# Performance work log

Hardware: AMD Instinct MI355X
Metric: run time of the kernel (lower is better)

The kernel has to match this reference:

```python
import jax, jax.numpy as jnp
import numpy as np

D_IN = 1024
D_OUT = 1024
N, S = 4, 2048

def setup_inputs() -> dict:
    key = jax.random.key(0)
    kv, kk, kq, k1, k2, k3 = jax.random.split(key, 6)
    return {
        "v": jax.random.normal(kv, (N, S, D_IN), dtype=jnp.float32),
        "k": jax.random.normal(kk, (N, S, D_IN), dtype=jnp.float32),
        "q": jax.random.normal(kq, (N, S, D_IN), dtype=jnp.float32),
        "WV": jax.random.normal(k1, (D_OUT, D_IN), dtype=jnp.float32),
        "WQ": jax.random.normal(k2, (D_OUT, D_IN), dtype=jnp.float32),
        "WK": jax.random.normal(k3, (D_OUT, D_IN), dtype=jnp.float32),
    }

def reference(v, k, q, WV, WQ, WK) -> jnp.ndarray:
    # projections: x @ W.T  -> [N, S, D_OUT]
    wv = jnp.einsum('nsw,ow->nso', v, WV)
    wk = jnp.einsum('nsw,ow->nso', k, WK)
    wq = jnp.einsum('nsw,ow->nso', q, WQ)
    # scores [N, Sq, Sk]; NOTE: softmax over axis=1 (query axis, matching torch dim=1),
    # then post-hoc division by input_shape[0] AFTER softmax (faithful to source).
    scores = jnp.einsum('nqo,nko->nqk', wq, wk)
    wqk = jax.nn.softmax(scores, axis=1) / jnp.float32(D_IN)
    return jnp.einsum('nqk,nko->nqo', wqk, wv)
```

## Files before the change

kernel.cpp:

```cpp
#include <hip/hip_runtime.h>
#include <math.h>


typedef _Float16 f16;
typedef _Float16 f16x8 __attribute__((ext_vector_type(8)));
typedef _Float16 f16x4 __attribute__((ext_vector_type(4)));
typedef float f32x4 __attribute__((ext_vector_type(4)));

enum StageMode { SM_PLANES2, SM_PLANES1 };
enum EpiMode   { EPI_F32, EPI_SPLIT, EPI_F16T };

#define GLL_PITCH 32

__device__ __forceinline__ void gll16(const f16* g, f16* l) {
    __builtin_amdgcn_global_load_lds(
        (const __attribute__((address_space(1))) void*)g,
        (__attribute__((address_space(3))) void*)l, 16, 0, 0);
}

__device__ __forceinline__ void stage_gll_plane(const f16* __restrict__ gplane,
                                                f16* __restrict__ lds,
                                                long rowBase, int ld, int k0,
                                                int wave, int lane)
{
#pragma unroll
    for (int i = 0; i < 2; i++) {
        int slotBase = (wave * 2 + i) * 64;
        int t = slotBase + lane;
        int r = t >> 2;
        int c = (t & 3) ^ ((r >> 1) & 3);
        const f16* g = gplane + (rowBase + r) * (long)ld + k0 + c * 8;
        gll16(g, lds + (long)slotBase * 8);
    }
}

__device__ __forceinline__ int frag_off_gll(int row, int g) {
    return row * GLL_PITCH + ((g ^ ((row >> 1) & 3)) << 3);
}

template<StageMode SA, StageMode SB, EpiMode EP, int GROUPM, bool STATS>
__global__ __launch_bounds__(256, 4)
void mfma_gemm(const f16* __restrict__ Ahi, const f16* __restrict__ Alo,
               const f16* __restrict__ Bhi, const f16* __restrict__ Blo,
               float* __restrict__ pmOut, float* __restrict__ psOut,
               void* __restrict__ C0, void* __restrict__ C1,
               int M, int Nc, int K, int lda, int ldb, int ldc,
               long batchA, long batchB, long batchC,
               float epiScale, int tsShift)
{
    constexpr bool TRIPLE = (SA == SM_PLANES2);
    constexpr int PLANE_SZ = 128 * GLL_PITCH;

    int bx, by;
    if constexpr (GROUPM > 0) {
        int gx = gridDim.x;
        int lin = blockIdx.y * gx + blockIdx.x;
        int nig = GROUPM * gx;
        int gid = lin / nig;
        int rem = lin - gid * nig;
        by = gid * GROUPM + (rem % GROUPM);
        bx = rem / GROUPM;
    } else {
        bx = blockIdx.x;
        by = blockIdx.y;
    }
    const int n0 = bx * 128;
    const int m0 = by * 128;
    const long z = blockIdx.z;

    const long aOfs = z * batchA, bOfs = z * batchB, cOfs = z * batchC;

    __shared__ __align__(16) f16 As_hi[PLANE_SZ];
    __shared__ __align__(16) f16 Bs_hi[PLANE_SZ];
    __shared__ __align__(16) f16 As_lo[TRIPLE ? PLANE_SZ : 8];
    __shared__ __align__(16) f16 Bs_lo[TRIPLE ? PLANE_SZ : 8];

    const int tid  = threadIdx.x;
    const int lane = tid & 63;
    const int wave = tid >> 6;
    const int wr = (wave >> 1) * 64;
    const int wc = (wave & 1) * 64;
    const int fm = lane & 15;
    const int fg = lane >> 4;

    f32x4 acc[4][4];
#pragma unroll
    for (int i = 0; i < 4; i++)
#pragma unroll
        for (int j = 0; j < 4; j++) acc[i][j] = (f32x4){0.f, 0.f, 0.f, 0.f};

    int roA[4], roB[4];
#pragma unroll
    for (int i = 0; i < 4; i++) {
        roA[i] = frag_off_gll(wr + i * 16 + fm, fg);
        roB[i] = frag_off_gll(wc + i * 16 + fm, fg);
    }

    for (int k0 = 0; k0 < K; k0 += 32) {
        stage_gll_plane(Ahi + aOfs, As_hi, m0, lda, k0, wave, lane);
        stage_gll_plane(Bhi + bOfs, Bs_hi, n0, ldb, k0, wave, lane);
        if constexpr (TRIPLE) {
            stage_gll_plane(Alo + aOfs, As_lo, m0, lda, k0, wave, lane);
            stage_gll_plane(Blo + bOfs, Bs_lo, n0, ldb, k0, wave, lane);
        }
        __syncthreads();

        f16x8 ah[4], bh[4], al[4], bl[4];
#pragma unroll
        for (int i = 0; i < 4; i++) {
            ah[i] = *(const f16x8*)&As_hi[roA[i]];
            bh[i] = *(const f16x8*)&Bs_hi[roB[i]];
            if constexpr (TRIPLE) {
                al[i] = *(const f16x8*)&As_lo[roA[i]];
                bl[i] = *(const f16x8*)&Bs_lo[roB[i]];
            }
        }
#pragma unroll
        for (int i = 0; i < 4; i++) {
#pragma unroll
            for (int j = 0; j < 4; j++) {
                acc[i][j] = __builtin_amdgcn_mfma_f32_16x16x32_f16(ah[i], bh[j], acc[i][j], 0, 0, 0);
                if constexpr (TRIPLE) {
                    acc[i][j] = __builtin_amdgcn_mfma_f32_16x16x32_f16(ah[i], bl[j], acc[i][j], 0, 0, 0);
                    acc[i][j] = __builtin_amdgcn_mfma_f32_16x16x32_f16(al[i], bh[j], acc[i][j], 0, 0, 0);
                }
            }
        }
        __syncthreads();
    }

    const int cr = fg * 4;
    const int cn = fm;
#pragma unroll
    for (int i = 0; i < 4; i++) {
#pragma unroll
        for (int j = 0; j < 4; j++) {
#pragma unroll
            for (int r = 0; r < 4; r++) {
                long mg = m0 + wr + i * 16 + cr + r;
                long ng = n0 + wc + j * 16 + cn;
                float val = acc[i][j][r] * epiScale;
                if constexpr (EP == EPI_F32) {
                    ((float*)C0)[cOfs + mg * ldc + ng] = val;
                } else if constexpr (EP == EPI_SPLIT) {
                    f16 h = (f16)val;
                    ((f16*)C0)[cOfs + mg * ldc + ng] = h;
                    ((f16*)C1)[cOfs + mg * ldc + ng] = (f16)(val - (float)h);
                } else {
                    long TS = 1L << tsShift;
                    long nb = mg >> tsShift;
                    long s  = mg & (TS - 1);
                    long addr = nb * ((long)Nc << tsShift) + ng * TS + s;
                    ((f16*)C0)[addr] = (f16)val;
                }
            }
        }
    }

    if constexpr (STATS) {
        __shared__ float stM[2][128];
        __shared__ float stS[2][128];
#pragma unroll
        for (int j = 0; j < 4; j++) {
            float mj = -3.402823466e38f;
#pragma unroll
            for (int i = 0; i < 4; i++)
#pragma unroll
                for (int r = 0; r < 4; r++) mj = fmaxf(mj, acc[i][j][r]);
            float sj = 0.f;
#pragma unroll
            for (int i = 0; i < 4; i++)
#pragma unroll
                for (int r = 0; r < 4; r++) sj += __expf(acc[i][j][r] - mj);
#pragma unroll
            for (int mask = 16; mask <= 32; mask <<= 1) {
                float mo = __shfl_xor(mj, mask, 64);
                float so = __shfl_xor(sj, mask, 64);
                float mn = fmaxf(mj, mo);
                sj = sj * __expf(mj - mn) + so * __expf(mo - mn);
                mj = mn;
            }
            if (fg == 0) {
                stM[wave >> 1][wc + j * 16 + cn] = mj;
                stS[wave >> 1][wc + j * 16 + cn] = sj;
            }
        }
        __syncthreads();
        if (tid < 128) {
            float ma = stM[0][tid], mb = stM[1][tid];
            float Mc = fmaxf(ma, mb);
            float Sv = stS[0][tid] * __expf(ma - Mc) + stS[1][tid] * __expf(mb - Mc);
            long o = ((long)z * (M >> 7) + by) * (long)Nc + (long)bx * 128 + tid;
            pmOut[o] = Mc;
            psOut[o] = Sv;
        }
    }
}

__global__ __launch_bounds__(512, 2)
void scores_gemm(const f16* __restrict__ Ahi, const f16* __restrict__ Alo,
                 const f16* __restrict__ Bhi, const f16* __restrict__ Blo,
                 float* __restrict__ pmOut, float* __restrict__ psOut,
                 float* __restrict__ C,
                 int M, int Nc, int K, int lda, int ldb, int ldc,
                 long batchA, long batchB, long batchC)
{
    constexpr int PLANE = 256 * GLL_PITCH;

    __shared__ __align__(16) f16 As_hi[2][PLANE];
    __shared__ __align__(16) f16 As_lo[2][PLANE];
    __shared__ __align__(16) f16 Bs_hi[2][PLANE];
    __shared__ __align__(16) f16 Bs_lo[2][PLANE];

    const int tid  = threadIdx.x;
    const int lane = tid & 63;
    const int wave = tid >> 6;
    const int rw   = wave >> 2;
    const int cw   = wave & 3;
    const int wrM  = rw * 128;
    const int wrN  = cw * 64;
    const int fm   = lane & 15;
    const int fg   = lane >> 4;

    const int n0 = blockIdx.x * 256;
    const int m0 = blockIdx.y * 256;
    const long z = blockIdx.z;
    const long aOfs = z * batchA, bOfs = z * batchB, cOfs = z * batchC;

    int slotBase[2], srcA[2], srcB[2];
#pragma unroll
    for (int i = 0; i < 2; i++) {
        int sb = (wave * 2 + i) * 64;
        int t  = sb + lane;
        int r  = t >> 2;
        int c  = (t & 3) ^ ((r >> 1) & 3);
        slotBase[i] = sb * 8;
        srcA[i] = (m0 + r) * lda + c * 8;
        srcB[i] = (n0 + r) * ldb + c * 8;
    }

#define SC_STAGE(buf, k0) do {                                              \
    _Pragma("unroll")                                                        \
    for (int s_ = 0; s_ < 2; s_++) {                                         \
        gll16(Ahi + aOfs + srcA[s_] + (k0), &As_hi[buf][slotBase[s_]]);      \
        gll16(Alo + aOfs + srcA[s_] + (k0), &As_lo[buf][slotBase[s_]]);      \
        gll16(Bhi + bOfs + srcB[s_] + (k0), &Bs_hi[buf][slotBase[s_]]);      \
        gll16(Blo + bOfs + srcB[s_] + (k0), &Bs_lo[buf][slotBase[s_]]);      \
    } } while (0)

    f32x4 acc[8][4];
#pragma unroll
    for (int i = 0; i < 8; i++)
#pragma unroll
        for (int j = 0; j < 4; j++) acc[i][j] = (f32x4){0.f, 0.f, 0.f, 0.f};

    int roA[8], roB[4];
#pragma unroll
    for (int i = 0; i < 8; i++) roA[i] = frag_off_gll(wrM + i * 16 + fm, fg);
#pragma unroll
    for (int j = 0; j < 4; j++) roB[j] = frag_off_gll(wrN + j * 16 + fm, fg);

    const int NT = K >> 5;
    SC_STAGE(0, 0);

    for (int t = 0; t < NT; t++) {
        const int cur = t & 1;
        __syncthreads();
        if (t + 1 < NT) SC_STAGE(cur ^ 1, (t + 1) * 32);

        f16x8 bh[4], bl[4];
#pragma unroll
        for (int j = 0; j < 4; j++) {
            bh[j] = *(const f16x8*)&Bs_hi[cur][roB[j]];
            bl[j] = *(const f16x8*)&Bs_lo[cur][roB[j]];
        }
#pragma unroll
        for (int h = 0; h < 2; h++) {
            f16x8 ah[4], al[4];
#pragma unroll
            for (int i = 0; i < 4; i++) {
                ah[i] = *(const f16x8*)&As_hi[cur][roA[h * 4 + i]];
                al[i] = *(const f16x8*)&As_lo[cur][roA[h * 4 + i]];
            }
            __builtin_amdgcn_s_setprio(1);
#pragma unroll
            for (int i = 0; i < 4; i++)
#pragma unroll
                for (int j = 0; j < 4; j++)
                    acc[h * 4 + i][j] = __builtin_amdgcn_mfma_f32_16x16x32_f16(
                        ah[i], bh[j], acc[h * 4 + i][j], 0, 0, 0);
#pragma unroll
            for (int i = 0; i < 4; i++)
#pragma unroll
                for (int j = 0; j < 4; j++)
                    acc[h * 4 + i][j] = __builtin_amdgcn_mfma_f32_16x16x32_f16(
                        ah[i], bl[j], acc[h * 4 + i][j], 0, 0, 0);
#pragma unroll
            for (int i = 0; i < 4; i++)
#pragma unroll
                for (int j = 0; j < 4; j++)
                    acc[h * 4 + i][j] = __builtin_amdgcn_mfma_f32_16x16x32_f16(
                        al[i], bh[j], acc[h * 4 + i][j], 0, 0, 0);
            __builtin_amdgcn_s_setprio(0);
        }
    }
#undef SC_STAGE

    const int cr = fg * 4;
#pragma unroll
    for (int i = 0; i < 8; i++) {
#pragma unroll
        for (int j = 0; j < 4; j++) {
#pragma unroll
            for (int r = 0; r < 4; r++) {
                long mg = m0 + wrM + i * 16 + cr + r;
                long ng = n0 + wrN + j * 16 + fm;
                C[cOfs + mg * (long)ldc + ng] = acc[i][j][r];
            }
        }
    }

    __shared__ float stM[2][256];
    __shared__ float stS[2][256];
#pragma unroll
    for (int j = 0; j < 4; j++) {
        float mj = -3.402823466e38f;
#pragma unroll
        for (int i = 0; i < 8; i++)
#pragma unroll
            for (int r = 0; r < 4; r++) mj = fmaxf(mj, acc[i][j][r]);
        float sj = 0.f;
#pragma unroll
        for (int i = 0; i < 8; i++)
#pragma unroll
            for (int r = 0; r < 4; r++) sj += __expf(acc[i][j][r] - mj);
#pragma unroll
        for (int mask = 16; mask <= 32; mask <<= 1) {
            float mo = __shfl_xor(mj, mask, 64);
            float so = __shfl_xor(sj, mask, 64);
            float mn = fmaxf(mj, mo);
            sj = sj * __expf(mj - mn) + so * __expf(mo - mn);
            mj = mn;
        }
        if (fg == 0) {
            stM[rw][wrN + j * 16 + fm] = mj;
            stS[rw][wrN + j * 16 + fm] = sj;
        }
    }
    __syncthreads();
    if (tid < 256) {
        float ma = stM[0][tid], mb = stM[1][tid];
        float Mc = fmaxf(ma, mb);
        float Sv = stS[0][tid] * __expf(ma - Mc) + stS[1][tid] * __expf(mb - Mc);
        long o = ((long)z * (M >> 8) + blockIdx.y) * (long)Nc + (long)blockIdx.x * 256 + tid;
        pmOut[o] = Mc;
        psOut[o] = Sv;
    }
}

template<bool HAS_LO>
__global__ __launch_bounds__(256)
void split_kernel(const float* __restrict__ src, f16* __restrict__ hi,
                  f16* __restrict__ lo, long n)
{
    long i = ((long)blockIdx.x * 256 + threadIdx.x) * 8;
    if (i >= n) return;
    float4 x0 = *(const float4*)&src[i];
    float4 x1 = *(const float4*)&src[i + 4];
    float xs[8] = {x0.x, x0.y, x0.z, x0.w, x1.x, x1.y, x1.z, x1.w};
    f16x8 h, l;
#pragma unroll
    for (int e = 0; e < 8; e++) {
        f16 hh = (f16)xs[e];
        h[e] = hh;
        if (HAS_LO) l[e] = (f16)(xs[e] - (float)hh);
    }
    *(f16x8*)&hi[i] = h;
    if (HAS_LO) *(f16x8*)&lo[i] = l;
}

template<int CH>
__global__ __launch_bounds__(64)
void stats_combine_kernel(const float* __restrict__ pm, const float* __restrict__ ps,
                          float* __restrict__ statM, float* __restrict__ statR, int S)
{
    const int n = blockIdx.y;
    const int kk = blockIdx.x * 64 + threadIdx.x;
    float M = -INFINITY;
#pragma unroll
    for (int i = 0; i < CH; i++)
        M = fmaxf(M, pm[((long)n * CH + i) * S + kk]);
    float Ssum = 0.f;
#pragma unroll
    for (int i = 0; i < CH; i++)
        Ssum += ps[((long)n * CH + i) * S + kk] * __expf(pm[((long)n * CH + i) * S + kk] - M);
    statM[(long)n * S + kk] = M;
    statR[(long)n * S + kk] = 1.0f / Ssum;
}

__global__ __launch_bounds__(256)
void pmat_kernel(const float* __restrict__ Sc, const float* __restrict__ statM,
                 const float* __restrict__ statR, f16* __restrict__ Phi, int S)
{
    const int n = blockIdx.z;
    const int kk = blockIdx.x * 1024 + threadIdx.x * 4;
    const float* Sn = Sc + (long)n * S * S;
    f16* ph = Phi + (long)n * S * S;
    float4 M4 = *(const float4*)&statM[(long)n * S + kk];
    float4 R4 = *(const float4*)&statR[(long)n * S + kk];
    const int q0 = blockIdx.y * 32;
    for (int qi = 0; qi < 32; qi++) {
        long idx = (long)(q0 + qi) * S + kk;
        float4 x = *(const float4*)&Sn[idx];
        f16x4 p;
        p[0] = (f16)(__expf(x.x - M4.x) * R4.x);
        p[1] = (f16)(__expf(x.y - M4.y) * R4.y);
        p[2] = (f16)(__expf(x.z - M4.z) * R4.z);
        p[3] = (f16)(__expf(x.w - M4.w) * R4.w);
        *(f16x4*)&ph[idx] = p;
    }
}

extern "C" void kernel_launch(void* const* d_in, const int* in_sizes, int n_in,
                              void* d_out, int out_size, void* d_ws, size_t ws_size,
                              hipStream_t stream)
{
    const float* v  = (const float*)d_in[0];
    const float* k  = (const float*)d_in[1];
    const float* q  = (const float*)d_in[2];
    const float* WV = (const float*)d_in[3];
    const float* WQ = (const float*)d_in[4];
    const float* WK = (const float*)d_in[5];
    float* out = (float*)d_out;

    const int N = 4, S = 2048, D = 1024;
    const long NSD = (long)N * S * D;
    const long DD  = (long)D * D;

    f16* ws = (f16*)d_ws;
    f16* q_hi = ws;
    f16* q_lo = ws + NSD;
    f16* k_hi = ws + 2 * NSD;
    f16* k_lo = ws + 3 * NSD;
    f16* v_hi = ws + 4 * NSD;
    f16* Wb   = ws + 5 * NSD;
    f16* WQ_hi = Wb,          *WQ_lo = Wb + DD;
    f16* WK_hi = Wb + 2 * DD, *WK_lo = Wb + 3 * DD;
    f16* WV_hi = Wb + 4 * DD;
    f16* wq_hi = ws + 5 * NSD + 5 * DD;
    f16* wq_lo = wq_hi + NSD;
    f16* wk_hi = wq_hi + 2 * NSD;
    f16* wk_lo = wq_hi + 3 * NSD;
    f16* wvT_hi = ws;
    float* Sc   = (float*)(ws + NSD);
    f16* P_hi   = wq_hi;
    float* pm    = (float*)(ws + 9 * NSD + 5 * DD);
    float* ps    = pm + (long)N * 8 * S;
    float* statM = ps + (long)N * 8 * S;
    float* statR = statM + (long)N * S;

    dim3 blk(256);

    split_kernel<true ><<<dim3(NSD / 2048), blk, 0, stream>>>(q,  q_hi, q_lo, NSD);
    split_kernel<true ><<<dim3(NSD / 2048), blk, 0, stream>>>(k,  k_hi, k_lo, NSD);
    split_kernel<false><<<dim3(NSD / 2048), blk, 0, stream>>>(v,  v_hi, nullptr, NSD);
    split_kernel<true ><<<dim3(DD / 2048),  blk, 0, stream>>>(WQ, WQ_hi, WQ_lo, DD);
    split_kernel<true ><<<dim3(DD / 2048),  blk, 0, stream>>>(WK, WK_hi, WK_lo, DD);
    split_kernel<false><<<dim3(DD / 2048),  blk, 0, stream>>>(WV, WV_hi, nullptr, DD);

    {
        dim3 g(D / 128, (N * S) / 128, 1);
        mfma_gemm<SM_PLANES2, SM_PLANES2, EPI_SPLIT, 4, false><<<g, blk, 0, stream>>>(
            q_hi, q_lo, WQ_hi, WQ_lo, nullptr, nullptr, wq_hi, wq_lo,
            N * S, D, D, D, D, D, 0, 0, 0, 1.0f, 0);
        mfma_gemm<SM_PLANES2, SM_PLANES2, EPI_SPLIT, 4, false><<<g, blk, 0, stream>>>(
            k_hi, k_lo, WK_hi, WK_lo, nullptr, nullptr, wk_hi, wk_lo,
            N * S, D, D, D, D, D, 0, 0, 0, 1.0f, 0);
        mfma_gemm<SM_PLANES1, SM_PLANES1, EPI_F16T, 4, false><<<g, blk, 0, stream>>>(
            v_hi, nullptr, WV_hi, nullptr, nullptr, nullptr, wvT_hi, nullptr,
            N * S, D, D, D, D, 0, 0, 0, 0, 1.0f, 11 );
    }
    {
        dim3 g(S / 256, S / 256, N);
        scores_gemm<<<g, dim3(512), 0, stream>>>(
            wq_hi, wq_lo, wk_hi, wk_lo, pm, ps, Sc,
            S, S, D, D, D, S, (long)S * D, (long)S * D, (long)S * S);
    }
    {
        dim3 gB(S / 64, N);
        stats_combine_kernel<8><<<gB, dim3(64), 0, stream>>>(pm, ps, statM, statR, S);
    }
    {
        dim3 g(S / 1024, S / 32, N);
        pmat_kernel<<<g, blk, 0, stream>>>(Sc, statM, statR, P_hi, S);
    }
    {
        dim3 g(D / 128, S / 128, N);
        mfma_gemm<SM_PLANES1, SM_PLANES1, EPI_F32, 4, false><<<g, blk, 0, stream>>>(
            P_hi, nullptr, wvT_hi, nullptr, nullptr, nullptr, out, nullptr,
            S, D, S, S, S, D, (long)S * S, (long)S * D, (long)S * D, 1.0f / (float)D, 0);
    }
}
```

Measured before the change: 472.8 us.

## Prefetch two stages ahead with vmcnt waits and remap blocks across XCDs

Restructures the scores GEMM main loop so two K-stages are in flight at once. Explicit vmcnt waits and raw s_barrier calls replace the blanket __syncthreads, and the next stage is issued into the current buffer after the A fragments for the second half are read. It also remaps the linear block id so each XCD gets a contiguous set of tiles sharing batch and row, aiming at better L2 reuse. The mapping hardcodes an 8x8x4 grid, and the vmcnt(8) count relies on exactly eight loads per stage.

```diff
diff --git a/kernel.cpp b/kernel.cpp
--- a/kernel.cpp
+++ b/kernel.cpp
@@ -222,9 +222,17 @@
     const int fm   = lane & 15;
     const int fg   = lane >> 4;
 
-    const int n0 = blockIdx.x * 256;
-    const int m0 = blockIdx.y * 256;
-    const long z = blockIdx.z;
+    const int Lid = (int)(blockIdx.z * 64 + blockIdx.y * 8 + blockIdx.x);
+    const int xcd = Lid & 7;
+    const int sct = Lid >> 3;
+    const int bxn = sct & 7;
+    const int idxp = xcd * 4 + (sct >> 3);
+    const int byn = idxp & 7;
+    const int zn  = idxp >> 3;
+
+    const int n0 = bxn * 256;
+    const int m0 = byn * 256;
+    const long z = zn;
     const long aOfs = z * batchA, bOfs = z * batchB, cOfs = z * batchC;
 
     int slotBase[2], srcA[2], srcB[2];
@@ -262,47 +270,78 @@
 
     const int NT = K >> 5;
     SC_STAGE(0, 0);
+    SC_STAGE(1, 32);
 
     for (int t = 0; t < NT; t++) {
         const int cur = t & 1;
-        __syncthreads();
-        if (t + 1 < NT) SC_STAGE(cur ^ 1, (t + 1) * 32);
-
-        f16x8 bh[4], bl[4];
+        if (t < NT - 1) {
+            asm volatile("s_waitcnt vmcnt(8)" ::: "memory");
+        } else {
+            asm volatile("s_waitcnt vmcnt(0)" ::: "memory");
+        }
+        __builtin_amdgcn_sched_barrier(0);
+        __builtin_amdgcn_s_barrier();
+        __builtin_amdgcn_sched_barrier(0);
+
+        f16x8 bh[4], bl[4], a0h[4], a0l[4];
 #pragma unroll
         for (int j = 0; j < 4; j++) {
             bh[j] = *(const f16x8*)&Bs_hi[cur][roB[j]];
             bl[j] = *(const f16x8*)&Bs_lo[cur][roB[j]];
         }
 #pragma unroll
-        for (int h = 0; h < 2; h++) {
-            f16x8 ah[4], al[4];
-#pragma unroll
-            for (int i = 0; i < 4; i++) {
-                ah[i] = *(const f16x8*)&As_hi[cur][roA[h * 4 + i]];
-                al[i] = *(const f16x8*)&As_lo[cur][roA[h * 4 + i]];
-            }
-            __builtin_amdgcn_s_setprio(1);
-#pragma unroll
-            for (int i = 0; i < 4; i++)
-#pragma unroll
-                for (int j = 0; j < 4; j++)
-                    acc[h * 4 + i][j] = __builtin_amdgcn_mfma_f32_16x16x32_f16(
-                        ah[i], bh[j], acc[h * 4 + i][j], 0, 0, 0);
-#pragma unroll
-            for (int i = 0; i < 4; i++)
-#pragma unroll
-                for (int j = 0; j < 4; j++)
-                    acc[h * 4 + i][j] = __builtin_amdgcn_mfma_f32_16x16x32_f16(
-                        ah[i], bl[j], acc[h * 4 + i][j], 0, 0, 0);
-#pragma unroll
-            for (int i = 0; i < 4; i++)
-#pragma unroll
-                for (int j = 0; j < 4; j++)
-                    acc[h * 4 + i][j] = __builtin_amdgcn_mfma_f32_16x16x32_f16(
-                        al[i], bh[j], acc[h * 4 + i][j], 0, 0, 0);
-            __builtin_amdgcn_s_setprio(0);
-        }
+        for (int i = 0; i < 4; i++) {
+            a0h[i] = *(const f16x8*)&As_hi[cur][roA[i]];
+            a0l[i] = *(const f16x8*)&As_lo[cur][roA[i]];
+        }
+        __builtin_amdgcn_s_setprio(1);
+#pragma unroll
+        for (int i = 0; i < 4; i++)
+#pragma unroll
+            for (int j = 0; j < 4; j++)
+                acc[i][j] = __builtin_amdgcn_mfma_f32_16x16x32_f16(a0h[i], bh[j], acc[i][j], 0, 0, 0);
+#pragma unroll
+        for (int i = 0; i < 4; i++)
+#pragma unroll
+            for (int j = 0; j < 4; j++)
+                acc[i][j] = __builtin_amdgcn_mfma_f32_16x16x32_f16(a0h[i], bl[j], acc[i][j], 0, 0, 0);
+#pragma unroll
+        for (int i = 0; i < 4; i++)
+#pragma unroll
+            for (int j = 0; j < 4; j++)
+                acc[i][j] = __builtin_amdgcn_mfma_f32_16x16x32_f16(a0l[i], bh[j], acc[i][j], 0, 0, 0);
+        __builtin_amdgcn_s_setprio(0);
+
+        f16x8 a1h[4], a1l[4];
+#pragma unroll
+        for (int i = 0; i < 4; i++) {
+            a1h[i] = *(const f16x8*)&As_hi[cur][roA[4 + i]];
+            a1l[i] = *(const f16x8*)&As_lo[cur][roA[4 + i]];
+        }
+        asm volatile("s_waitcnt lgkmcnt(0)" ::: "memory");
+        __builtin_amdgcn_sched_barrier(0);
+        __builtin_amdgcn_s_barrier();
+        __builtin_amdgcn_sched_barrier(0);
+
+        if (t + 2 < NT) SC_STAGE(cur, (t + 2) * 32);
+
+        __builtin_amdgcn_s_setprio(1);
+#pragma unroll
+        for (int i = 0; i < 4; i++)
+#pragma unroll
+            for (int j = 0; j < 4; j++)
+                acc[4 + i][j] = __builtin_amdgcn_mfma_f32_16x16x32_f16(a1h[i], bh[j], acc[4 + i][j], 0, 0, 0);
+#pragma unroll
+        for (int i = 0; i < 4; i++)
+#pragma unroll
+            for (int j = 0; j < 4; j++)
+                acc[4 + i][j] = __builtin_amdgcn_mfma_f32_16x16x32_f16(a1h[i], bl[j], acc[4 + i][j], 0, 0, 0);
+#pragma unroll
+        for (int i = 0; i < 4; i++)
+#pragma unroll
+            for (int j = 0; j < 4; j++)
+                acc[4 + i][j] = __builtin_amdgcn_mfma_f32_16x16x32_f16(a1l[i], bh[j], acc[4 + i][j], 0, 0, 0);
+        __builtin_amdgcn_s_setprio(0);
     }
 #undef SC_STAGE
 
@@ -352,7 +391,7 @@
         float ma = stM[0][tid], mb = stM[1][tid];
         float Mc = fmaxf(ma, mb);
         float Sv = stS[0][tid] * __expf(ma - Mc) + stS[1][tid] * __expf(mb - Mc);
-        long o = ((long)z * (M >> 8) + blockIdx.y) * (long)Nc + (long)blockIdx.x * 256 + tid;
+        long o = ((long)z * (M >> 8) + byn) * (long)Nc + (long)bxn * 256 + tid;
         pmOut[o] = Mc;
         psOut[o] = Sv;
     }
```

Measured after the change: 459.0 us. 2.9% less time.
